# Kernel tuning notes

Measured on AMD Instinct MI355X. Metric: run time of the kernel, lower is better.

The kernel has to match this reference:

```python
import jax, jax.numpy as jnp
import numpy as np

DIM = 512   # model dim C (num_heads=1 -> head_dim = C)
NK = 128    # tokens per key-batch element
BQ = 512    # query batch
BK = 256    # key batch
NC = 1000   # num_classes for visual_fc head


def _ln(x, g, b, eps=1e-5):
    m = x.mean(-1, keepdims=True)
    v = x.var(-1, keepdims=True)
    return (x - m) * jax.lax.rsqrt(v + eps) * g + b


def _l2norm(x, eps=1e-12):  # F.normalize(p=2, dim=-1)
    n = jnp.linalg.norm(x, axis=-1, keepdims=True)
    return x / jnp.maximum(n, eps)


def setup_inputs() -> dict:
    key = jax.random.key(0)
    ks = jax.random.split(key, 8)
    s = 0.02
    return {
        "qx": jax.random.normal(ks[0], (BQ, 1, DIM), dtype=jnp.float32),
        "kx": jax.random.normal(ks[1], (BK, NK, DIM), dtype=jnp.float32),
        "key_padding_mask": jax.random.randint(ks[2], (BK, NK), 0, 2).astype(bool),
        "logit_scale": jnp.array([np.log(100.0)], dtype=jnp.float32),
        "g_q": jnp.ones((DIM,), jnp.float32), "b_q": jnp.zeros((DIM,), jnp.float32),
        "g_k": jnp.ones((DIM,), jnp.float32), "b_k": jnp.zeros((DIM,), jnp.float32),
        "wq": jax.random.normal(ks[3], (DIM, DIM), dtype=jnp.float32) * s,
        "wk": jax.random.normal(ks[4], (DIM, DIM), dtype=jnp.float32) * s,
        "w1": jax.random.normal(ks[5], (4 * DIM, DIM), dtype=jnp.float32) * s,
        "b1": jnp.zeros((4 * DIM,), jnp.float32),
        "w2": jax.random.normal(ks[6], (NC, 4 * DIM), dtype=jnp.float32) * s,
        "b2": jnp.zeros((NC,), jnp.float32),
    }


def reference(qx, kx, key_padding_mask, logit_scale,
              g_q, b_q, g_k, b_k, wq, wk, w1, b1, w2, b2):
    C = qx.shape[-1]
    scale = C ** -0.5  # num_heads=1 so head_dim == C
    # cross-batch single-query attention (Attention.forward)
    q = _ln(qx, g_q, b_q) @ wq.T                       # [Bq,1,C]
    k = _ln(kx, g_k, b_k) @ wk.T                       # [Bk,Nk,C]
    attn = jnp.einsum('qoc,knc->qkn', q, k) * scale    # [Bq,Bk,Nk]
    attn = jnp.where(key_padding_mask[None, :, :], -jnp.inf, attn)
    attn = jax.nn.softmax(attn, axis=-1)
    v = jnp.einsum('knc,qkn->qkc', kx, attn)           # [Bq,Bk,C]
    # two_branch head
    h = jax.nn.relu(qx[:, 0, :] @ w1.T + b1)           # [Bq,4C]
    x1 = h @ w2.T + b2                                 # [Bq,NC]
    x2 = jnp.einsum('qkc,qoc->qk', _l2norm(v), _l2norm(qx)) * jnp.exp(logit_scale)[0]
    return (x1, x2)
```

## Files before the change

### kernel.cpp

```cpp
#include <hip/hip_runtime.h>

typedef unsigned short u16;
typedef unsigned int u32;
typedef short bf16x8s __attribute__((ext_vector_type(8)));
typedef float f32x4 __attribute__((ext_vector_type(4)));

#define SCALE_C 0.044194173824159216f
#define MFMA16 __builtin_amdgcn_mfma_f32_16x16x32_bf16

__device__ __forceinline__ u16 f2bf(float f){
  union { float f; u32 u; } c; c.f = f;
  u32 u = c.u;
  return (u16)((u + 0x7fffu + ((u >> 16) & 1u)) >> 16);
}

__device__ __forceinline__ void gload16(const void* g, void* l){
  __builtin_amdgcn_global_load_lds((const __attribute__((address_space(1))) void*)g,
                                   (__attribute__((address_space(3))) void*)l, 16, 0, 0);
}

#define OFF_KXB  ((size_t)0)
#define OFF_G    (OFF_KXB + 33554432)
#define OFF_W2B  (OFF_G + 8388608)
#define OFF_H    (OFF_W2B + 4096000)
#define OFF_W1B  (OFF_H + 2097152)
#define OFF_QLN  (OFF_W1B + 2097152)
#define OFF_QHAT (OFF_QLN + 524288)
#define OFF_QXB  (OFF_QHAT + 524288)
#define OFF_P    (OFF_QXB + 524288)
#define OFF_M2   (OFF_P + 524288)
#define OFF_WQB  (OFF_M2 + 524288)
#define OFF_WCT  (OFF_WQB + 524288)
#define OFF_KM   (OFF_WCT + 524288)
#define OFF_KR   (OFF_KM + 131072)
#define OFF_T2   (OFF_KR + 131072)
#define OFF_FLAG (OFF_T2 + 4096)

__global__ __launch_bounds__(512) void k_phase1(
    const float* __restrict__ qx, const float* __restrict__ kx,
    const int* __restrict__ maskw,
    const float* __restrict__ g_q, const float* __restrict__ b_q,
    const float* __restrict__ wq, const float* __restrict__ wk,
    const float* __restrict__ w1, const float* __restrict__ b1,
    const float* __restrict__ w2, const float* __restrict__ b2,
    u16* __restrict__ kxb, float* __restrict__ km, float* __restrict__ kr,
    u16* __restrict__ Gm,
    u16* __restrict__ qln, u16* __restrict__ qhat,
    u16* __restrict__ wct, u16* __restrict__ w2b, u16* __restrict__ hbuf,
    float* __restrict__ t2s, int* __restrict__ flag, float* __restrict__ x1o)
{
  __shared__ __align__(16) u16 lBig[16384];
  __shared__ float redq[8][2];
  __shared__ int smax;
  const int bid = blockIdx.x, tid = threadIdx.x;
  const int lane = tid & 63, w = tid >> 6;
  const int l15 = lane & 15, lg = lane >> 4;

  if (bid < 256){
    u16* lk = lBig;
    const int z = bid;
    const int a0 = (w>>2)*64, b0 = (w&3)*32;
    float s[16] = {0,0,0,0,0,0,0,0,0,0,0,0,0,0,0,0};
    float sq[16] = {0,0,0,0,0,0,0,0,0,0,0,0,0,0,0,0};
    f32x4 acc[4][2] = {};
    for (int ch = 0; ch < 4; ch++){
      #pragma unroll
      for (int i = 0; i < 16; i++){
        int r = w*16 + i;
        float2 v = *(const float2*)(kx + ((size_t)z*128 + r)*512 + ch*128 + lane*2);
        s[i] += v.x + v.y; sq[i] += v.x*v.x + v.y*v.y;
        u32 pk = f2bf(v.x) | ((u32)f2bf(v.y)<<16);
        *(u32*)(kxb + ((size_t)z*128 + r)*512 + ch*128 + lane*2) = pk;
        *(u32*)&lk[r*128 + ((lane*2) ^ ((r&7)<<3))] = pk;
      }
      __syncthreads();
      #pragma unroll
      for (int kk = 0; kk < 4; kk++){
        int cgr = kk*4 + lg;
        bf16x8s a[4], b[2];
        #pragma unroll
        for (int i2 = 0; i2 < 4; i2++){
          int r = a0 + i2*16 + l15;
          a[i2] = *(const bf16x8s*)&lk[r*128 + ((cgr*8) ^ ((r&7)<<3))];
        }
        #pragma unroll
        for (int j = 0; j < 2; j++){
          int r = b0 + j*16 + l15;
          b[j] = *(const bf16x8s*)&lk[r*128 + ((cgr*8) ^ ((r&7)<<3))];
        }
        #pragma unroll
        for (int i2 = 0; i2 < 4; i2++)
          #pragma unroll
          for (int j = 0; j < 2; j++)
            acc[i2][j] = MFMA16(a[i2], b[j], acc[i2][j], 0,0,0);
      }
      __syncthreads();
    }
    #pragma unroll
    for (int i = 0; i < 16; i++){
      float ss = s[i], qq = sq[i];
      #pragma unroll
      for (int o = 1; o < 64; o <<= 1){ ss += __shfl_xor(ss,o); qq += __shfl_xor(qq,o); }
      if (lane == 0){
        int r = w*16 + i;
        float mean = ss*(1.0f/512.0f);
        float var  = qq*(1.0f/512.0f) - mean*mean;
        km[z*128+r] = mean; kr[z*128+r] = rsqrtf(var + 1e-5f);
      }
    }
    u16* G = Gm + (size_t)z*16384;
    #pragma unroll
    for (int i2 = 0; i2 < 4; i2++)
      #pragma unroll
      for (int j = 0; j < 2; j++)
        #pragma unroll
        for (int r = 0; r < 4; r++)
          G[(size_t)(a0 + i2*16 + lg*4 + r)*128 + b0 + j*16 + l15] = f2bf(acc[i2][j][r]);
  } else if (bid < 512){
    const int row = (bid-256)*2 + (tid>>8);
    const int t = tid & 255;
    float2 v = *(const float2*)(qx + (size_t)row*512 + t*2);
    float s = v.x+v.y, sq = v.x*v.x+v.y*v.y;
    #pragma unroll
    for (int o = 1; o < 64; o <<= 1){ s += __shfl_xor(s,o); sq += __shfl_xor(sq,o); }
    if (lane == 0){ redq[w][0]=s; redq[w][1]=sq; }
    __syncthreads();
    const int h4 = (tid>>8)*4;
    s  = redq[h4][0]+redq[h4+1][0]+redq[h4+2][0]+redq[h4+3][0];
    sq = redq[h4][1]+redq[h4+1][1]+redq[h4+2][1]+redq[h4+3][1];
    float mean = s*(1.0f/512.0f);
    float var  = sq*(1.0f/512.0f) - mean*mean;
    float rstd = rsqrtf(var + 1e-5f);
    float il2  = 1.0f / fmaxf(sqrtf(sq), 1e-12f);
    float2 g  = *(const float2*)(g_q + t*2);
    float2 bb = *(const float2*)(b_q + t*2);
    u32 a  = f2bf((v.x-mean)*rstd*g.x+bb.x) | ((u32)f2bf((v.y-mean)*rstd*g.y+bb.y)<<16);
    u32 hh = f2bf(v.x*il2) | ((u32)f2bf(v.y*il2)<<16);
    *(u32*)(qln  + (size_t)row*512 + t*2) = a;
    *(u32*)(qhat + (size_t)row*512 + t*2) = hh;
  } else if (bid < 1512){
    int i = (bid-512)*512 + tid;
    float4 v = *(const float4*)(w2 + (size_t)i*4);
    uint2 p;
    p.x = f2bf(v.x)|((u32)f2bf(v.y)<<16); p.y = f2bf(v.z)|((u32)f2bf(v.w)<<16);
    *(uint2*)(w2b + (size_t)i*4) = p;
  } else if (bid < 1640){
    const int t = bid - 1512;
    const int m0 = (t >> 4)*64, n0 = (t & 15)*128;
    const int w4 = w & 3;
    const int nb = (w >> 2)*64;
    const int wr = (w4>>1)*32, wc = (w4&1)*32;
    u16* shA = lBig;
    u16* shB = lBig + 4096;
    f32x4 acc[2][2] = {};
    for (int kc = 0; kc < 512; kc += 64){
      {
        int row = tid >> 3, c8 = (tid & 7)*8;
        float4 a0 = *(const float4*)(qx + (size_t)(m0+row)*512 + kc + c8);
        float4 a1 = *(const float4*)(qx + (size_t)(m0+row)*512 + kc + c8 + 4);
        u16 ta[8] = {f2bf(a0.x),f2bf(a0.y),f2bf(a0.z),f2bf(a0.w),
                     f2bf(a1.x),f2bf(a1.y),f2bf(a1.z),f2bf(a1.w)};
        *(uint4*)&shA[row*64 + (((tid&7) ^ (row&7))*8)] = *(uint4*)ta;
        #pragma unroll
        for (int s2 = 0; s2 < 2; s2++){
          int u = tid + s2*512;
          int rowb = u >> 3, cb8 = (u & 7)*8;
          float4 b0 = *(const float4*)(w1 + (size_t)(n0+rowb)*512 + kc + cb8);
          float4 b1v = *(const float4*)(w1 + (size_t)(n0+rowb)*512 + kc + cb8 + 4);
          u16 tb[8] = {f2bf(b0.x),f2bf(b0.y),f2bf(b0.z),f2bf(b0.w),
                       f2bf(b1v.x),f2bf(b1v.y),f2bf(b1v.z),f2bf(b1v.w)};
          *(uint4*)&shB[rowb*64 + (((u&7) ^ (rowb&7))*8)] = *(uint4*)tb;
        }
      }
      __syncthreads();
      #pragma unroll
      for (int kk = 0; kk < 2; kk++){
        int cgr = kk*4 + lg;
        int ra0 = wr + l15, ra1 = wr + 16 + l15;
        int rb0 = nb + wc + l15, rb1 = nb + wc + 16 + l15;
        bf16x8s a0 = *(const bf16x8s*)&shA[ra0*64 + ((cgr ^ (ra0&7))*8)];
        bf16x8s a1 = *(const bf16x8s*)&shA[ra1*64 + ((cgr ^ (ra1&7))*8)];
        bf16x8s b0 = *(const bf16x8s*)&shB[rb0*64 + ((cgr ^ (rb0&7))*8)];
        bf16x8s b1 = *(const bf16x8s*)&shB[rb1*64 + ((cgr ^ (rb1&7))*8)];
        acc[0][0]=MFMA16(a0,b0,acc[0][0],0,0,0);
        acc[0][1]=MFMA16(a0,b1,acc[0][1],0,0,0);
        acc[1][0]=MFMA16(a1,b0,acc[1][0],0,0,0);
        acc[1][1]=MFMA16(a1,b1,acc[1][1],0,0,0);
      }
      __syncthreads();
    }
    #pragma unroll
    for (int i = 0; i < 2; i++)
      #pragma unroll
      for (int j = 0; j < 2; j++){
        int col = n0 + nb + wc + j*16 + l15;
        float bv = b1[col];
        #pragma unroll
        for (int r = 0; r < 4; r++){
          int row = m0 + wr + i*16 + lg*4 + r;
          hbuf[(size_t)row*2048 + col] = f2bf(fmaxf(acc[i][j][r] + bv, 0.0f));
        }
      }
  } else if (bid < 1704){
    const int t = bid - 1640;
    const int f0 = (t>>3)*64, c0 = (t&7)*64;
    const int w4 = w & 3;
    const int wr = (w4>>1)*32, wc = (w4&1)*32;
    u16* shA = lBig;
    u16* shB = lBig + 4096;
    f32x4 acc[2][2] = {};
    for (int i0 = 0; i0 < 512; i0 += 64){
      const int ii = tid >> 3;
      const int cc8 = (tid & 7) * 8;
      float4 va0 = *(const float4*)(wk + (size_t)(i0+ii)*512 + f0 + cc8);
      float4 va1 = *(const float4*)(wk + (size_t)(i0+ii)*512 + f0 + cc8 + 4);
      float4 vb0 = *(const float4*)(wq + (size_t)(i0+ii)*512 + c0 + cc8);
      float4 vb1 = *(const float4*)(wq + (size_t)(i0+ii)*512 + c0 + cc8 + 4);
      #pragma unroll
      for (int e = 0; e < 8; e++){
        float fa = e < 4 ? (&va0.x)[e] : (&va1.x)[e-4];
        float fb = e < 4 ? (&vb0.x)[e] : (&vb1.x)[e-4];
        int rowc = cc8 + e;
        int idx = rowc*64 + (((ii>>3) ^ (rowc&7))*8 + (ii&7));
        shA[idx] = f2bf(fa);
        shB[idx] = f2bf(fb);
      }
      __syncthreads();
      #pragma unroll
      for (int kk = 0; kk < 2; kk++){
        int cgr = kk*4 + lg;
        int ra0 = wr + l15, ra1 = wr + 16 + l15;
        int rb0 = wc + l15, rb1 = wc + 16 + l15;
        bf16x8s a0 = *(const bf16x8s*)&shA[ra0*64 + ((cgr ^ (ra0&7))*8)];
        bf16x8s a1 = *(const bf16x8s*)&shA[ra1*64 + ((cgr ^ (ra1&7))*8)];
        bf16x8s b0 = *(const bf16x8s*)&shB[rb0*64 + ((cgr ^ (rb0&7))*8)];
        bf16x8s b1 = *(const bf16x8s*)&shB[rb1*64 + ((cgr ^ (rb1&7))*8)];
        acc[0][0]=MFMA16(a0,b0,acc[0][0],0,0,0);
        acc[0][1]=MFMA16(a0,b1,acc[0][1],0,0,0);
        acc[1][0]=MFMA16(a1,b0,acc[1][0],0,0,0);
        acc[1][1]=MFMA16(a1,b1,acc[1][1],0,0,0);
      }
      __syncthreads();
    }
    if (tid < 256){
      #pragma unroll
      for (int i = 0; i < 2; i++)
        #pragma unroll
        for (int j = 0; j < 2; j++)
          #pragma unroll
          for (int r = 0; r < 4; r++)
            wct[(size_t)(f0 + wr + i*16 + lg*4 + r)*512 + c0 + wc + j*16 + l15]
                = f2bf(acc[i][j][r]);
    }
  } else if (bid < 1954){
    int i = (bid-1704)*2048 + tid*4;
    #pragma unroll
    for (int e = 0; e < 4; e++){
      int idx = i + e;
      x1o[idx] = b2[idx % 1000];
    }
  } else {
    if (tid == 0) smax = 0;
    t2s[tid] = 0.0f;
    __syncthreads();
    int mx = 0;
    for (int i = tid; i < 8192; i += 512){ int v = maskw[i]; mx = v > mx ? v : mx; }
    #pragma unroll
    for (int o = 1; o < 64; o <<= 1){ int t2 = __shfl_xor(mx,o); mx = t2 > mx ? t2 : mx; }
    if ((tid & 63) == 0) atomicMax(&smax, mx);
    __syncthreads();
    if (tid == 0) *flag = (smax <= 1) ? 1 : 0;
  }
}

__device__ __forceinline__ void gemm_body(const u16* __restrict__ Ap, const u16* __restrict__ Bp,
    int M, int N, int K, int m0, int n0, int tid,
    u16 (*lA)[64], u16 (*lB)[64], f32x4 (&acc)[2][2])
{
  const int lane = tid & 63, w = tid >> 6;
  const int wr = (w >> 1)*32, wc = (w & 1)*32;
  const int l15 = lane & 15, lg = lane >> 4;
  for (int kc = 0; kc < K; kc += 64){
    #pragma unroll
    for (int s = 0; s < 2; s++){
      int u = tid + s*256;
      int row = u >> 3, cg = u & 7;
      int sw = (cg ^ (row & 7)) * 8;
      uint4 va = make_uint4(0,0,0,0);
      if (m0 + row < M) va = *(const uint4*)(Ap + (size_t)(m0+row)*K + kc + cg*8);
      *(uint4*)&lA[row][sw] = va;
      uint4 vb = make_uint4(0,0,0,0);
      if (n0 + row < N) vb = *(const uint4*)(Bp + (size_t)(n0+row)*K + kc + cg*8);
      *(uint4*)&lB[row][sw] = vb;
    }
    __syncthreads();
    #pragma unroll
    for (int kk = 0; kk < 2; kk++){
      int cgr = kk*4 + lg;
      int ra0 = wr + l15, ra1 = wr + 16 + l15;
      int rb0 = wc + l15, rb1 = wc + 16 + l15;
      bf16x8s a0 = *(const bf16x8s*)&lA[ra0][(cgr ^ (ra0&7))*8];
      bf16x8s a1 = *(const bf16x8s*)&lA[ra1][(cgr ^ (ra1&7))*8];
      bf16x8s b0 = *(const bf16x8s*)&lB[rb0][(cgr ^ (rb0&7))*8];
      bf16x8s b1 = *(const bf16x8s*)&lB[rb1][(cgr ^ (rb1&7))*8];
      acc[0][0] = MFMA16(a0,b0,acc[0][0],0,0,0);
      acc[0][1] = MFMA16(a0,b1,acc[0][1],0,0,0);
      acc[1][0] = MFMA16(a1,b0,acc[1][0],0,0,0);
      acc[1][1] = MFMA16(a1,b1,acc[1][1],0,0,0);
    }
    __syncthreads();
  }
}

__global__ __launch_bounds__(256) void k_phase2(
    const u16* __restrict__ qln, const u16* __restrict__ wct,
    const float* __restrict__ g_k, u16* __restrict__ m2, float* __restrict__ t2s,
    const u16* __restrict__ hbuf, const u16* __restrict__ w2b,
    float* __restrict__ x1o)
{
  __shared__ __align__(16) u16 lA[64][64], lB[64][64];
  f32x4 acc[2][2] = {};
  const int bid = blockIdx.x, tid = threadIdx.x;
  const int lane = tid & 63, w = tid >> 6;
  const int wr = (w >> 1)*32, wc = (w & 1)*32;
  const int l15 = lane & 15, lg = lane >> 4;
  if (bid < 512){
    const int ks = bid >> 7;
    const int t  = bid & 127;
    const int m0 = (t >> 4)*64, n0 = (t & 15)*64;
    for (int kc = ks*512; kc < ks*512 + 512; kc += 64){
      #pragma unroll
      for (int s = 0; s < 2; s++){
        int u = tid + s*256;
        int row = u >> 3, cg = u & 7;
        int sw = (cg ^ (row & 7)) * 8;
        *(uint4*)&lA[row][sw] = *(const uint4*)(hbuf + (size_t)(m0+row)*2048 + kc + cg*8);
        uint4 vb = make_uint4(0,0,0,0);
        if (n0 + row < 1000) vb = *(const uint4*)(w2b + (size_t)(n0+row)*2048 + kc + cg*8);
        *(uint4*)&lB[row][sw] = vb;
      }
      __syncthreads();
      #pragma unroll
      for (int kk = 0; kk < 2; kk++){
        int cgr = kk*4 + lg;
        int ra0 = wr + l15, ra1 = wr + 16 + l15;
        int rb0 = wc + l15, rb1 = wc + 16 + l15;
        bf16x8s a0 = *(const bf16x8s*)&lA[ra0][(cgr ^ (ra0&7))*8];
        bf16x8s a1 = *(const bf16x8s*)&lA[ra1][(cgr ^ (ra1&7))*8];
        bf16x8s b0 = *(const bf16x8s*)&lB[rb0][(cgr ^ (rb0&7))*8];
        bf16x8s b1 = *(const bf16x8s*)&lB[rb1][(cgr ^ (rb1&7))*8];
        acc[0][0]=MFMA16(a0,b0,acc[0][0],0,0,0);
        acc[0][1]=MFMA16(a0,b1,acc[0][1],0,0,0);
        acc[1][0]=MFMA16(a1,b0,acc[1][0],0,0,0);
        acc[1][1]=MFMA16(a1,b1,acc[1][1],0,0,0);
      }
      __syncthreads();
    }
    #pragma unroll
    for (int i = 0; i < 2; i++)
      #pragma unroll
      for (int j = 0; j < 2; j++){
        int col = n0 + wc + j*16 + l15;
        if (col < 1000){
          #pragma unroll
          for (int r = 0; r < 4; r++){
            int row = m0 + wr + i*16 + lg*4 + r;
            atomicAdd(&x1o[(size_t)row*1000 + col], acc[i][j][r]);
          }
        }
      }
  } else {
    const int b = bid - 512;
    int m0 = (b>>3)*64, n0 = (b&7)*64;
    gemm_body(qln, wct, 512,512,512, m0,n0, tid, lA, lB, acc);
    #pragma unroll
    for (int i = 0; i < 2; i++){
      #pragma unroll
      for (int r = 0; r < 4; r++){
        int row = m0 + wr + i*16 + lg*4 + r;
        float part = 0.f;
        #pragma unroll
        for (int j = 0; j < 2; j++){
          int col = n0 + wc + j*16 + l15;
          float e = SCALE_C * acc[i][j][r] * g_k[col];
          m2[(size_t)row*512 + col] = f2bf(e);
          part += e;
        }
        #pragma unroll
        for (int o = 1; o < 16; o <<= 1) part += __shfl_xor(part, o);
        if (l15 == 0) atomicAdd(&t2s[row], part);
      }
    }
  }
}

__global__ __launch_bounds__(512, 4) void k_attn(
    const u16* __restrict__ kxb, const u16* __restrict__ Gm,
    const u16* __restrict__ m2, const u16* __restrict__ qhat,
    const float* __restrict__ km, const float* __restrict__ kr,
    const float* __restrict__ t2s, const void* __restrict__ maskp,
    const int* __restrict__ flagp, const float* __restrict__ lsp,
    float* __restrict__ x2)
{
  __shared__ __align__(16) u16 sb[24576];
  __shared__ float lt2[128];
  __shared__ float lNum[128][2], lDen[128][2];
  u16* lP = sb;

  const int kb = blockIdx.x, q0 = blockIdx.y * 128;
  const int tid = threadIdx.x, lane = tid & 63, w = tid >> 6;
  const int wr = (w >> 1)*32, wcol = (w & 1)*64;
  const int l15 = lane & 15, lg = lane >> 4;
  const int fl = *flagp;
  const float expls = __expf(lsp[0]);

  if (tid < 128) lt2[tid] = t2s[q0 + tid];

  float kmv[4], krv[4], mbv[4];
  #pragma unroll
  for (int j = 0; j < 4; j++){
    int gn = kb*128 + wcol + j*16 + l15;
    kmv[j] = km[gn]; krv[j] = kr[gn];
    int mv = fl ? ((const int*)maskp)[gn] : (int)((const unsigned char*)maskp)[gn];
    mbv[j] = mv ? -1e30f : 0.0f;
  }

  const u16* KX = kxb + (size_t)kb * 65536;
  f32x4 aS[2][4] = {}, aD[2][4] = {};

  const int srow  = w*16 + (lane >> 2);
  const int sslot = (lane & 3) ^ ((srow >> 1) & 3);
  const int lofs  = w*512;

  #define STAGE(p) do{                                                         \
    const int kc_ = (p)*32;                                                    \
    u16* b_ = sb + ((p)&1)*12288;                                              \
    gload16(KX   + (size_t)srow*512      + kc_ + sslot*8, b_ + lofs);          \
    gload16(m2   + (size_t)(q0+srow)*512 + kc_ + sslot*8, b_ + 4096 + lofs);   \
    gload16(qhat + (size_t)(q0+srow)*512 + kc_ + sslot*8, b_ + 8192 + lofs);   \
  }while(0)

  STAGE(0);
  #pragma unroll
  for (int p = 0; p < 16; p++){
    if (p < 15){
      STAGE(p+1);
      asm volatile("s_waitcnt vmcnt(3)" ::: "memory");
    } else {
      asm volatile("s_waitcnt vmcnt(0)" ::: "memory");
    }
    __builtin_amdgcn_s_barrier();
    __builtin_amdgcn_sched_barrier(0);
    const u16* lb  = sb + (p&1)*12288;
    const u16* lKX = lb;
    const u16* lM2 = lb + 4096;
    const u16* lQH = lb + 8192;
    const int rA0 = wr + l15, rA1 = wr + 16 + l15;
    bf16x8s am0 = *(const bf16x8s*)&lM2[rA0*32 + ((lg ^ ((rA0>>1)&3))*8)];
    bf16x8s am1 = *(const bf16x8s*)&lM2[rA1*32 + ((lg ^ ((rA1>>1)&3))*8)];
    bf16x8s aq0 = *(const bf16x8s*)&lQH[rA0*32 + ((lg ^ ((rA0>>1)&3))*8)];
    bf16x8s aq1 = *(const bf16x8s*)&lQH[rA1*32 + ((lg ^ ((rA1>>1)&3))*8)];
    __builtin_amdgcn_s_setprio(1);
    #pragma unroll
    for (int j = 0; j < 4; j++){
      int rB = wcol + j*16 + l15;
      bf16x8s bk = *(const bf16x8s*)&lKX[rB*32 + ((lg ^ ((rB>>1)&3))*8)];
      aS[0][j] = MFMA16(am0, bk, aS[0][j], 0,0,0);
      aS[1][j] = MFMA16(am1, bk, aS[1][j], 0,0,0);
      aD[0][j] = MFMA16(aq0, bk, aD[0][j], 0,0,0);
      aD[1][j] = MFMA16(aq1, bk, aD[1][j], 0,0,0);
    }
    __builtin_amdgcn_s_setprio(0);
    __builtin_amdgcn_sched_barrier(0);
    __builtin_amdgcn_s_barrier();
  }
  __syncthreads();

  #pragma unroll
  for (int i = 0; i < 2; i++){
    #pragma unroll
    for (int r = 0; r < 4; r++){
      int rowl = wr + i*16 + lg*4 + r;
      float t2v = lt2[rowl];
      float sn = 0.f;
      #pragma unroll
      for (int j = 0; j < 4; j++){
        float L = krv[j]*(aS[i][j][r] - kmv[j]*t2v) + mbv[j];
        float e = __expf(L);
        aS[i][j][r] = e;
        sn += e * aD[i][j][r];
      }
      #pragma unroll
      for (int o = 1; o < 16; o <<= 1) sn += __shfl_xor(sn, o);
      if (l15 == 0) lNum[rowl][w&1] = sn;
      #pragma unroll
      for (int j = 0; j < 4; j++){
        int n = wcol + j*16 + l15;
        lP[rowl*128 + ((n>>3)^(rowl&7))*8 + (n&7)] = f2bf(aS[i][j][r]);
      }
    }
  }
  __syncthreads();

  f32x4 aT[2][4] = {};
  const u16* Gk = Gm + (size_t)kb * 16384;
  #pragma unroll
  for (int kk = 0; kk < 4; kk++){
    int cgr = kk*4 + lg;
    int rA0 = wr + l15, rA1 = wr + 16 + l15;
    bf16x8s p0 = *(const bf16x8s*)&lP[rA0*128 + ((cgr^(rA0&7))*8)];
    bf16x8s p1 = *(const bf16x8s*)&lP[rA1*128 + ((cgr^(rA1&7))*8)];
    #pragma unroll
    for (int j = 0; j < 4; j++){
      int mcol = wcol + j*16 + l15;
      bf16x8s bg = *(const bf16x8s*)(Gk + (size_t)mcol*128 + kk*32 + lg*8);
      aT[0][j] = MFMA16(p0, bg, aT[0][j], 0,0,0);
      aT[1][j] = MFMA16(p1, bg, aT[1][j], 0,0,0);
    }
  }
  #pragma unroll
  for (int i = 0; i < 2; i++){
    #pragma unroll
    for (int r = 0; r < 4; r++){
      int rowl = wr + i*16 + lg*4 + r;
      float sd = 0.f;
      #pragma unroll
      for (int j = 0; j < 4; j++) sd += aT[i][j][r] * aS[i][j][r];
      #pragma unroll
      for (int o = 1; o < 16; o <<= 1) sd += __shfl_xor(sd, o);
      if (l15 == 0) lDen[rowl][w&1] = sd;
    }
  }
  __syncthreads();

  if (tid < 128){
    float num  = lNum[tid][0] + lNum[tid][1];
    float den2 = lDen[tid][0] + lDen[tid][1];
    float den  = fmaxf(sqrtf(fmaxf(den2, 0.0f)), 1e-12f);
    x2[(size_t)(q0 + tid)*256 + kb] = expls * num / den;
  }
}

extern "C" void kernel_launch(void* const* d_in, const int* in_sizes, int n_in,
                              void* d_out, int out_size, void* d_ws, size_t ws_size,
                              hipStream_t stream)
{
  (void)in_sizes; (void)n_in; (void)out_size; (void)ws_size;
  const float* qx  = (const float*)d_in[0];
  const float* kx  = (const float*)d_in[1];
  const void*  mask= d_in[2];
  const float* lsp = (const float*)d_in[3];
  const float* g_q = (const float*)d_in[4];
  const float* b_q = (const float*)d_in[5];
  const float* g_k = (const float*)d_in[6];
  const float* wq  = (const float*)d_in[8];
  const float* wk  = (const float*)d_in[9];
  const float* w1  = (const float*)d_in[10];
  const float* b1  = (const float*)d_in[11];
  const float* w2  = (const float*)d_in[12];
  const float* b2  = (const float*)d_in[13];

  char* ws = (char*)d_ws;
  u16* kxb  = (u16*)(ws + OFF_KXB);
  u16* Gm   = (u16*)(ws + OFF_G);
  u16* w2b  = (u16*)(ws + OFF_W2B);
  u16* hbuf = (u16*)(ws + OFF_H);
  u16* qln  = (u16*)(ws + OFF_QLN);
  u16* qhat = (u16*)(ws + OFF_QHAT);
  u16* m2   = (u16*)(ws + OFF_M2);
  u16* wct  = (u16*)(ws + OFF_WCT);
  float* km  = (float*)(ws + OFF_KM);
  float* kr  = (float*)(ws + OFF_KR);
  float* t2s = (float*)(ws + OFF_T2);
  int*   flag= (int*)(ws + OFF_FLAG);
  float* x1o = (float*)d_out;
  float* x2o = (float*)d_out + 512*1000;

  k_phase1<<<dim3(1955), dim3(512), 0, stream>>>(
      qx, kx, (const int*)mask, g_q, b_q, wq, wk, w1, b1, w2, b2,
      kxb, km, kr, Gm, qln, qhat, wct, w2b, hbuf, t2s, flag, x1o);
  k_phase2<<<dim3(576), dim3(256), 0, stream>>>(
      qln, wct, g_k, m2, t2s, hbuf, w2b, x1o);
  k_attn<<<dim3(256, 4), dim3(512), 0, stream>>>(
      kxb, Gm, m2, qhat, km, kr, t2s, mask, flag, lsp, x2o);
}
```

Measured before the change: 121.3 us.

## Rebalance kernel stages: move small GEMMs earlier, fuse x1 GEMM into attention launch

```diff
diff --git a/kernel.cpp b/kernel.cpp
--- a/kernel.cpp
+++ b/kernel.cpp
@@ -36,20 +36,15 @@
 #define OFF_T2   (OFF_KR + 131072)
 #define OFF_FLAG (OFF_T2 + 4096)
 
-__global__ __launch_bounds__(512) void k_phase1(
-    const float* __restrict__ qx, const float* __restrict__ kx,
-    const int* __restrict__ maskw,
+__global__ __launch_bounds__(512) void k_phase0(
+    const float* __restrict__ qx, const int* __restrict__ maskw,
     const float* __restrict__ g_q, const float* __restrict__ b_q,
     const float* __restrict__ wq, const float* __restrict__ wk,
-    const float* __restrict__ w1, const float* __restrict__ b1,
-    const float* __restrict__ w2, const float* __restrict__ b2,
-    u16* __restrict__ kxb, float* __restrict__ km, float* __restrict__ kr,
-    u16* __restrict__ Gm,
-    u16* __restrict__ qln, u16* __restrict__ qhat,
-    u16* __restrict__ wct, u16* __restrict__ w2b, u16* __restrict__ hbuf,
+    const float* __restrict__ b2,
+    u16* __restrict__ qln, u16* __restrict__ qhat, u16* __restrict__ wct,
     float* __restrict__ t2s, int* __restrict__ flag, float* __restrict__ x1o)
 {
-  __shared__ __align__(16) u16 lBig[16384];
+  __shared__ __align__(16) u16 lBig[8192];
   __shared__ float redq[8][2];
   __shared__ int smax;
   const int bid = blockIdx.x, tid = threadIdx.x;
@@ -57,67 +52,7 @@
   const int l15 = lane & 15, lg = lane >> 4;
 
   if (bid < 256){
-    u16* lk = lBig;
-    const int z = bid;
-    const int a0 = (w>>2)*64, b0 = (w&3)*32;
-    float s[16] = {0,0,0,0,0,0,0,0,0,0,0,0,0,0,0,0};
-    float sq[16] = {0,0,0,0,0,0,0,0,0,0,0,0,0,0,0,0};
-    f32x4 acc[4][2] = {};
-    for (int ch = 0; ch < 4; ch++){
-      #pragma unroll
-      for (int i = 0; i < 16; i++){
-        int r = w*16 + i;
-        float2 v = *(const float2*)(kx + ((size_t)z*128 + r)*512 + ch*128 + lane*2);
-        s[i] += v.x + v.y; sq[i] += v.x*v.x + v.y*v.y;
-        u32 pk = f2bf(v.x) | ((u32)f2bf(v.y)<<16);
-        *(u32*)(kxb + ((size_t)z*128 + r)*512 + ch*128 + lane*2) = pk;
-        *(u32*)&lk[r*128 + ((lane*2) ^ ((r&7)<<3))] = pk;
-      }
-      __syncthreads();
-      #pragma unroll
-      for (int kk = 0; kk < 4; kk++){
-        int cgr = kk*4 + lg;
-        bf16x8s a[4], b[2];
-        #pragma unroll
-        for (int i2 = 0; i2 < 4; i2++){
-          int r = a0 + i2*16 + l15;
-          a[i2] = *(const bf16x8s*)&lk[r*128 + ((cgr*8) ^ ((r&7)<<3))];
-        }
-        #pragma unroll
-        for (int j = 0; j < 2; j++){
-          int r = b0 + j*16 + l15;
-          b[j] = *(const bf16x8s*)&lk[r*128 + ((cgr*8) ^ ((r&7)<<3))];
-        }
-        #pragma unroll
-        for (int i2 = 0; i2 < 4; i2++)
-          #pragma unroll
-          for (int j = 0; j < 2; j++)
-            acc[i2][j] = MFMA16(a[i2], b[j], acc[i2][j], 0,0,0);
-      }
-      __syncthreads();
-    }
-    #pragma unroll
-    for (int i = 0; i < 16; i++){
-      float ss = s[i], qq = sq[i];
-      #pragma unroll
-      for (int o = 1; o < 64; o <<= 1){ ss += __shfl_xor(ss,o); qq += __shfl_xor(qq,o); }
-      if (lane == 0){
-        int r = w*16 + i;
-        float mean = ss*(1.0f/512.0f);
-        float var  = qq*(1.0f/512.0f) - mean*mean;
-        km[z*128+r] = mean; kr[z*128+r] = rsqrtf(var + 1e-5f);
-      }
-    }
-    u16* G = Gm + (size_t)z*16384;
-    #pragma unroll
-    for (int i2 = 0; i2 < 4; i2++)
-      #pragma unroll
-      for (int j = 0; j < 2; j++)
-        #pragma unroll
-        for (int r = 0; r < 4; r++)
-          G[(size_t)(a0 + i2*16 + lg*4 + r)*128 + b0 + j*16 + l15] = f2bf(acc[i2][j][r]);
-  } else if (bid < 512){
-    const int row = (bid-256)*2 + (tid>>8);
+    const int row = bid*2 + (tid>>8);
     const int t = tid & 255;
     float2 v = *(const float2*)(qx + (size_t)row*512 + t*2);
     float s = v.x+v.y, sq = v.x*v.x+v.y*v.y;
@@ -138,14 +73,154 @@
     u32 hh = f2bf(v.x*il2) | ((u32)f2bf(v.y*il2)<<16);
     *(u32*)(qln  + (size_t)row*512 + t*2) = a;
     *(u32*)(qhat + (size_t)row*512 + t*2) = hh;
-  } else if (bid < 1512){
-    int i = (bid-512)*512 + tid;
-    float4 v = *(const float4*)(w2 + (size_t)i*4);
-    uint2 p;
-    p.x = f2bf(v.x)|((u32)f2bf(v.y)<<16); p.y = f2bf(v.z)|((u32)f2bf(v.w)<<16);
-    *(uint2*)(w2b + (size_t)i*4) = p;
-  } else if (bid < 1640){
-    const int t = bid - 1512;
+  } else if (bid < 320){
+    const int t = bid - 256;
+    const int f0 = (t>>3)*64, c0 = (t&7)*64;
+    const int w4 = w & 3;
+    const int wr = (w4>>1)*32, wc = (w4&1)*32;
+    u16* shA = lBig;
+    u16* shB = lBig + 4096;
+    f32x4 acc[2][2] = {};
+    for (int i0 = 0; i0 < 512; i0 += 64){
+      const int ii = tid >> 3;
+      const int cc8 = (tid & 7) * 8;
+      float4 va0 = *(const float4*)(wk + (size_t)(i0+ii)*512 + f0 + cc8);
+      float4 va1 = *(const float4*)(wk + (size_t)(i0+ii)*512 + f0 + cc8 + 4);
+      float4 vb0 = *(const float4*)(wq + (size_t)(i0+ii)*512 + c0 + cc8);
+      float4 vb1 = *(const float4*)(wq + (size_t)(i0+ii)*512 + c0 + cc8 + 4);
+      #pragma unroll
+      for (int e = 0; e < 8; e++){
+        float fa = e < 4 ? (&va0.x)[e] : (&va1.x)[e-4];
+        float fb = e < 4 ? (&vb0.x)[e] : (&vb1.x)[e-4];
+        int rowc = cc8 + e;
+        int idx = rowc*64 + (((ii>>3) ^ (rowc&7))*8 + (ii&7));
+        shA[idx] = f2bf(fa);
+        shB[idx] = f2bf(fb);
+      }
+      __syncthreads();
+      #pragma unroll
+      for (int kk = 0; kk < 2; kk++){
+        int cgr = kk*4 + lg;
+        int ra0 = wr + l15, ra1 = wr + 16 + l15;
+        int rb0 = wc + l15, rb1 = wc + 16 + l15;
+        bf16x8s a0 = *(const bf16x8s*)&shA[ra0*64 + ((cgr ^ (ra0&7))*8)];
+        bf16x8s a1 = *(const bf16x8s*)&shA[ra1*64 + ((cgr ^ (ra1&7))*8)];
+        bf16x8s b0 = *(const bf16x8s*)&shB[rb0*64 + ((cgr ^ (rb0&7))*8)];
+        bf16x8s b1 = *(const bf16x8s*)&shB[rb1*64 + ((cgr ^ (rb1&7))*8)];
+        acc[0][0]=MFMA16(a0,b0,acc[0][0],0,0,0);
+        acc[0][1]=MFMA16(a0,b1,acc[0][1],0,0,0);
+        acc[1][0]=MFMA16(a1,b0,acc[1][0],0,0,0);
+        acc[1][1]=MFMA16(a1,b1,acc[1][1],0,0,0);
+      }
+      __syncthreads();
+    }
+    if (tid < 256){
+      #pragma unroll
+      for (int i = 0; i < 2; i++)
+        #pragma unroll
+        for (int j = 0; j < 2; j++)
+          #pragma unroll
+          for (int r = 0; r < 4; r++)
+            wct[(size_t)(f0 + wr + i*16 + lg*4 + r)*512 + c0 + wc + j*16 + l15]
+                = f2bf(acc[i][j][r]);
+    }
+  } else if (bid < 570){
+    int i = (bid-320)*2048 + tid*4;
+    #pragma unroll
+    for (int e = 0; e < 4; e++){
+      int idx = i + e;
+      x1o[idx] = b2[idx % 1000];
+    }
+  } else {
+    if (tid == 0) smax = 0;
+    t2s[tid] = 0.0f;
+    __syncthreads();
+    int mx = 0;
+    for (int i = tid; i < 8192; i += 512){ int v = maskw[i]; mx = v > mx ? v : mx; }
+    #pragma unroll
+    for (int o = 1; o < 64; o <<= 1){ int t2 = __shfl_xor(mx,o); mx = t2 > mx ? t2 : mx; }
+    if ((tid & 63) == 0) atomicMax(&smax, mx);
+    __syncthreads();
+    if (tid == 0) *flag = (smax <= 1) ? 1 : 0;
+  }
+}
+
+__global__ __launch_bounds__(512) void k_phase1(
+    const float* __restrict__ qx, const float* __restrict__ kx,
+    const float* __restrict__ w1, const float* __restrict__ b1,
+    const u16* __restrict__ qln, const u16* __restrict__ wct,
+    const float* __restrict__ g_k,
+    u16* __restrict__ kxb, float* __restrict__ km, float* __restrict__ kr,
+    u16* __restrict__ Gm, u16* __restrict__ hbuf,
+    u16* __restrict__ m2, float* __restrict__ t2s)
+{
+  __shared__ __align__(16) u16 lBig[16384];
+  const int bid = blockIdx.x, tid = threadIdx.x;
+  const int lane = tid & 63, w = tid >> 6;
+  const int l15 = lane & 15, lg = lane >> 4;
+
+  if (bid < 256){
+    u16* lk = lBig;
+    const int z = bid;
+    const int a0 = (w>>2)*64, b0 = (w&3)*32;
+    float s[16] = {0,0,0,0,0,0,0,0,0,0,0,0,0,0,0,0};
+    float sq[16] = {0,0,0,0,0,0,0,0,0,0,0,0,0,0,0,0};
+    f32x4 acc[4][2] = {};
+    for (int ch = 0; ch < 4; ch++){
+      #pragma unroll
+      for (int i = 0; i < 16; i++){
+        int r = w*16 + i;
+        float2 v = *(const float2*)(kx + ((size_t)z*128 + r)*512 + ch*128 + lane*2);
+        s[i] += v.x + v.y; sq[i] += v.x*v.x + v.y*v.y;
+        u32 pk = f2bf(v.x) | ((u32)f2bf(v.y)<<16);
+        *(u32*)(kxb + ((size_t)z*128 + r)*512 + ch*128 + lane*2) = pk;
+        *(u32*)&lk[r*128 + ((lane*2) ^ ((r&7)<<3))] = pk;
+      }
+      __syncthreads();
+      #pragma unroll
+      for (int kk = 0; kk < 4; kk++){
+        int cgr = kk*4 + lg;
+        bf16x8s a[4], b[2];
+        #pragma unroll
+        for (int i2 = 0; i2 < 4; i2++){
+          int r = a0 + i2*16 + l15;
+          a[i2] = *(const bf16x8s*)&lk[r*128 + ((cgr*8) ^ ((r&7)<<3))];
+        }
+        #pragma unroll
+        for (int j = 0; j < 2; j++){
+          int r = b0 + j*16 + l15;
+          b[j] = *(const bf16x8s*)&lk[r*128 + ((cgr*8) ^ ((r&7)<<3))];
+        }
+        #pragma unroll
+        for (int i2 = 0; i2 < 4; i2++)
+          #pragma unroll
+          for (int j = 0; j < 2; j++)
+            acc[i2][j] = MFMA16(a[i2], b[j], acc[i2][j], 0,0,0);
+      }
+      __syncthreads();
+    }
+    #pragma unroll
+    for (int i = 0; i < 16; i++){
+      float ss = s[i], qq = sq[i];
+      #pragma unroll
+      for (int o = 1; o < 64; o <<= 1){ ss += __shfl_xor(ss,o); qq += __shfl_xor(qq,o); }
+      if (lane == 0){
+        int r = w*16 + i;
+        float mean = ss*(1.0f/512.0f);
+        float var  = qq*(1.0f/512.0f) - mean*mean;
+        km[z*128+r] = mean; kr[z*128+r] = rsqrtf(var + 1e-5f);
+      }
+    }
+    u16* G = Gm + (size_t)z*16384;
+    #pragma unroll
+    for (int i2 = 0; i2 < 4; i2++)
+      #pragma unroll
+      for (int j = 0; j < 2; j++)
+        #pragma unroll
+        for (int r = 0; r < 4; r++)
+          G[(size_t)(a0 + i2*16 + lg*4 + r)*128 + b0 + j*16 + l15] = f2bf(acc[i2][j][r]);
+  } else if (bid < 384){
+    const int t = bid - 256;
     const int m0 = (t >> 4)*64, n0 = (t & 15)*128;
     const int w4 = w & 3;
     const int nb = (w >> 2)*64;
@@ -201,29 +276,20 @@
           hbuf[(size_t)row*2048 + col] = f2bf(fmaxf(acc[i][j][r] + bv, 0.0f));
         }
       }
-  } else if (bid < 1704){
-    const int t = bid - 1640;
-    const int f0 = (t>>3)*64, c0 = (t&7)*64;
+  } else {
+    const int b = bid - 384;
+    const int m0 = (b>>3)*64, n0 = (b&7)*64;
     const int w4 = w & 3;
     const int wr = (w4>>1)*32, wc = (w4&1)*32;
     u16* shA = lBig;
     u16* shB = lBig + 4096;
     f32x4 acc[2][2] = {};
-    for (int i0 = 0; i0 < 512; i0 += 64){
-      const int ii = tid >> 3;
-      const int cc8 = (tid & 7) * 8;
-      float4 va0 = *(const float4*)(wk + (size_t)(i0+ii)*512 + f0 + cc8);
-      float4 va1 = *(const float4*)(wk + (size_t)(i0+ii)*512 + f0 + cc8 + 4);
-      float4 vb0 = *(const float4*)(wq + (size_t)(i0+ii)*512 + c0 + cc8);
-      float4 vb1 = *(const float4*)(wq + (size_t)(i0+ii)*512 + c0 + cc8 + 4);
-      #pragma unroll
-      for (int e = 0; e < 8; e++){
-        float fa = e < 4 ? (&va0.x)[e] : (&va1.x)[e-4];
-        float fb = e < 4 ? (&vb0.x)[e] : (&vb1.x)[e-4];
-        int rowc = cc8 + e;
-        int idx = rowc*64 + (((ii>>3) ^ (rowc&7))*8 + (ii&7));
-        shA[idx] = f2bf(fa);
-        shB[idx] = f2bf(fb);
+    for (int kc = 0; kc < 512; kc += 64){
+      {
+        int row = tid >> 3, cg = tid & 7;
+        int sw = (cg ^ (row & 7)) * 8;
+        *(uint4*)&shA[row*64 + sw] = *(const uint4*)(qln + (size_t)(m0+row)*512 + kc + cg*8);
+        *(uint4*)&shB[row*64 + sw] = *(const uint4*)(wct + (size_t)(n0+row)*512 + kc + cg*8);
       }
       __syncthreads();
       #pragma unroll
@@ -242,102 +308,74 @@
       }
       __syncthreads();
     }
-    if (tid < 256){
-      #pragma unroll
-      for (int i = 0; i < 2; i++)
-        #pragma unroll
-        for (int j = 0; j < 2; j++)
+    if (w < 4){
+      #pragma unroll
+      for (int i = 0; i < 2; i++){
+        #pragma unroll
+        for (int r = 0; r < 4; r++){
+          int row = m0 + wr + i*16 + lg*4 + r;
+          float part = 0.f;
           #pragma unroll
-          for (int r = 0; r < 4; r++)
-            wct[(size_t)(f0 + wr + i*16 + lg*4 + r)*512 + c0 + wc + j*16 + l15]
-                = f2bf(acc[i][j][r]);
-    }
-  } else if (bid < 1954){
-    int i = (bid-1704)*2048 + tid*4;
-    #pragma unroll
-    for (int e = 0; e < 4; e++){
-      int idx = i + e;
-      x1o[idx] = b2[idx % 1000];
-    }
-  } else {
-    if (tid == 0) smax = 0;
-    t2s[tid] = 0.0f;
-    __syncthreads();
-    int mx = 0;
-    for (int i = tid; i < 8192; i += 512){ int v = maskw[i]; mx = v > mx ? v : mx; }
-    #pragma unroll
-    for (int o = 1; o < 64; o <<= 1){ int t2 = __shfl_xor(mx,o); mx = t2 > mx ? t2 : mx; }
-    if ((tid & 63) == 0) atomicMax(&smax, mx);
-    __syncthreads();
-    if (tid == 0) *flag = (smax <= 1) ? 1 : 0;
+          for (int j = 0; j < 2; j++){
+            int col = n0 + wc + j*16 + l15;
+            float e = SCALE_C * acc[i][j][r] * g_k[col];
+            m2[(size_t)row*512 + col] = f2bf(e);
+            part += e;
+          }
+          #pragma unroll
+          for (int o = 1; o < 16; o <<= 1) part += __shfl_xor(part, o);
+          if (l15 == 0) atomicAdd(&t2s[row], part);
+        }
+      }
+    }
   }
 }
 
-__device__ __forceinline__ void gemm_body(const u16* __restrict__ Ap, const u16* __restrict__ Bp,
-    int M, int N, int K, int m0, int n0, int tid,
-    u16 (*lA)[64], u16 (*lB)[64], f32x4 (&acc)[2][2])
-{
-  const int lane = tid & 63, w = tid >> 6;
-  const int wr = (w >> 1)*32, wc = (w & 1)*32;
-  const int l15 = lane & 15, lg = lane >> 4;
-  for (int kc = 0; kc < K; kc += 64){
-    #pragma unroll
-    for (int s = 0; s < 2; s++){
-      int u = tid + s*256;
-      int row = u >> 3, cg = u & 7;
-      int sw = (cg ^ (row & 7)) * 8;
-      uint4 va = make_uint4(0,0,0,0);
-      if (m0 + row < M) va = *(const uint4*)(Ap + (size_t)(m0+row)*K + kc + cg*8);
-      *(uint4*)&lA[row][sw] = va;
-      uint4 vb = make_uint4(0,0,0,0);
-      if (n0 + row < N) vb = *(const uint4*)(Bp + (size_t)(n0+row)*K + kc + cg*8);
-      *(uint4*)&lB[row][sw] = vb;
-    }
-    __syncthreads();
-    #pragma unroll
-    for (int kk = 0; kk < 2; kk++){
-      int cgr = kk*4 + lg;
-      int ra0 = wr + l15, ra1 = wr + 16 + l15;
-      int rb0 = wc + l15, rb1 = wc + 16 + l15;
-      bf16x8s a0 = *(const bf16x8s*)&lA[ra0][(cgr ^ (ra0&7))*8];
-      bf16x8s a1 = *(const bf16x8s*)&lA[ra1][(cgr ^ (ra1&7))*8];
-      bf16x8s b0 = *(const bf16x8s*)&lB[rb0][(cgr ^ (rb0&7))*8];
-      bf16x8s b1 = *(const bf16x8s*)&lB[rb1][(cgr ^ (rb1&7))*8];
-      acc[0][0] = MFMA16(a0,b0,acc[0][0],0,0,0);
-      acc[0][1] = MFMA16(a0,b1,acc[0][1],0,0,0);
-      acc[1][0] = MFMA16(a1,b0,acc[1][0],0,0,0);
-      acc[1][1] = MFMA16(a1,b1,acc[1][1],0,0,0);
-    }
-    __syncthreads();
-  }
-}
-
-__global__ __launch_bounds__(256) void k_phase2(
-    const u16* __restrict__ qln, const u16* __restrict__ wct,
-    const float* __restrict__ g_k, u16* __restrict__ m2, float* __restrict__ t2s,
-    const u16* __restrict__ hbuf, const u16* __restrict__ w2b,
+__global__ __launch_bounds__(512, 4) void k_attn(
+    const u16* __restrict__ kxb, const u16* __restrict__ Gm,
+    const u16* __restrict__ m2, const u16* __restrict__ qhat,
+    const float* __restrict__ km, const float* __restrict__ kr,
+    const float* __restrict__ t2s, const void* __restrict__ maskp,
+    const int* __restrict__ flagp, const float* __restrict__ lsp,
+    float* __restrict__ x2,
+    const u16* __restrict__ hbuf, const float* __restrict__ w2,
     float* __restrict__ x1o)
 {
-  __shared__ __align__(16) u16 lA[64][64], lB[64][64];
-  f32x4 acc[2][2] = {};
-  const int bid = blockIdx.x, tid = threadIdx.x;
-  const int lane = tid & 63, w = tid >> 6;
-  const int wr = (w >> 1)*32, wc = (w & 1)*32;
+  __shared__ __align__(16) u16 sb[24576];
+  __shared__ float lt2[128];
+  __shared__ float lNum[128][2], lDen[128][2];
+  u16* lP = sb;
+
+  const int tid = threadIdx.x, lane = tid & 63, w = tid >> 6;
   const int l15 = lane & 15, lg = lane >> 4;
-  if (bid < 512){
-    const int ks = bid >> 7;
-    const int t  = bid & 127;
-    const int m0 = (t >> 4)*64, n0 = (t & 15)*64;
+
+  if (blockIdx.x < 64){
+    const int t = blockIdx.x*4 + blockIdx.y;
+    const int tile = t >> 2, ks = t & 3;
+    const int m0 = (tile>>3)*64, n0 = (tile&7)*128;
+    const int wr = (w >> 2)*32, wc = (w & 3)*32;
+    u16* lA = sb;
+    u16* lB = sb + 4096;
+    f32x4 acc[2][2] = {};
     for (int kc = ks*512; kc < ks*512 + 512; kc += 64){
-      #pragma unroll
-      for (int s = 0; s < 2; s++){
-        int u = tid + s*256;
-        int row = u >> 3, cg = u & 7;
-        int sw = (cg ^ (row & 7)) * 8;
-        *(uint4*)&lA[row][sw] = *(const uint4*)(hbuf + (size_t)(m0+row)*2048 + kc + cg*8);
-        uint4 vb = make_uint4(0,0,0,0);
-        if (n0 + row < 1000) vb = *(const uint4*)(w2b + (size_t)(n0+row)*2048 + kc + cg*8);
-        *(uint4*)&lB[row][sw] = vb;
+      {
+        int row = tid >> 3, cg = tid & 7;
+        *(uint4*)&lA[row*64 + ((cg ^ (row&7))*8)] =
+            *(const uint4*)(hbuf + (size_t)(m0+row)*2048 + kc + cg*8);
+        #pragma unroll
+        for (int s2 = 0; s2 < 2; s2++){
+          int u = tid + s2*512;
+          int rowb = u >> 3, cb8 = (u & 7)*8;
+          uint4 vb = make_uint4(0,0,0,0);
+          if (n0 + rowb < 1000){
+            float4 b0 = *(const float4*)(w2 + (size_t)(n0+rowb)*2048 + kc + cb8);
+            float4 b1v = *(const float4*)(w2 + (size_t)(n0+rowb)*2048 + kc + cb8 + 4);
+            u16 tb[8] = {f2bf(b0.x),f2bf(b0.y),f2bf(b0.z),f2bf(b0.w),
+                         f2bf(b1v.x),f2bf(b1v.y),f2bf(b1v.z),f2bf(b1v.w)};
+            vb = *(uint4*)tb;
+          }
+          *(uint4*)&lB[rowb*64 + (((u&7) ^ (rowb&7))*8)] = vb;
+        }
       }
       __syncthreads();
       #pragma unroll
@@ -345,10 +383,10 @@
         int cgr = kk*4 + lg;
         int ra0 = wr + l15, ra1 = wr + 16 + l15;
         int rb0 = wc + l15, rb1 = wc + 16 + l15;
-        bf16x8s a0 = *(const bf16x8s*)&lA[ra0][(cgr ^ (ra0&7))*8];
-        bf16x8s a1 = *(const bf16x8s*)&lA[ra1][(cgr ^ (ra1&7))*8];
-        bf16x8s b0 = *(const bf16x8s*)&lB[rb0][(cgr ^ (rb0&7))*8];
-        bf16x8s b1 = *(const bf16x8s*)&lB[rb1][(cgr ^ (rb1&7))*8];
+        bf16x8s a0 = *(const bf16x8s*)&lA[ra0*64 + ((cgr ^ (ra0&7))*8)];
+        bf16x8s a1 = *(const bf16x8s*)&lA[ra1*64 + ((cgr ^ (ra1&7))*8)];
+        bf16x8s b0 = *(const bf16x8s*)&lB[rb0*64 + ((cgr ^ (rb0&7))*8)];
+        bf16x8s b1 = *(const bf16x8s*)&lB[rb1*64 + ((cgr ^ (rb1&7))*8)];
         acc[0][0]=MFMA16(a0,b0,acc[0][0],0,0,0);
         acc[0][1]=MFMA16(a0,b1,acc[0][1],0,0,0);
         acc[1][0]=MFMA16(a1,b0,acc[1][0],0,0,0);
@@ -369,48 +407,11 @@
           }
         }
       }
-  } else {
-    const int b = bid - 512;
-    int m0 = (b>>3)*64, n0 = (b&7)*64;
-    gemm_body(qln, wct, 512,512,512, m0,n0, tid, lA, lB, acc);
-    #pragma unroll
-    for (int i = 0; i < 2; i++){
-      #pragma unroll
-      for (int r = 0; r < 4; r++){
-        int row = m0 + wr + i*16 + lg*4 + r;
-        float part = 0.f;
-        #pragma unroll
-        for (int j = 0; j < 2; j++){
-          int col = n0 + wc + j*16 + l15;
-          float e = SCALE_C * acc[i][j][r] * g_k[col];
-          m2[(size_t)row*512 + col] = f2bf(e);
-          part += e;
-        }
-        #pragma unroll
-        for (int o = 1; o < 16; o <<= 1) part += __shfl_xor(part, o);
-        if (l15 == 0) atomicAdd(&t2s[row], part);
-      }
-    }
-  }
-}
-
-__global__ __launch_bounds__(512, 4) void k_attn(
-    const u16* __restrict__ kxb, const u16* __restrict__ Gm,
-    const u16* __restrict__ m2, const u16* __restrict__ qhat,
-    const float* __restrict__ km, const float* __restrict__ kr,
-    const float* __restrict__ t2s, const void* __restrict__ maskp,
-    const int* __restrict__ flagp, const float* __restrict__ lsp,
-    float* __restrict__ x2)
-{
-  __shared__ __align__(16) u16 sb[24576];
-  __shared__ float lt2[128];
-  __shared__ float lNum[128][2], lDen[128][2];
-  u16* lP = sb;
-
-  const int kb = blockIdx.x, q0 = blockIdx.y * 128;
-  const int tid = threadIdx.x, lane = tid & 63, w = tid >> 6;
+    return;
+  }
+
+  const int kb = blockIdx.x - 64, q0 = blockIdx.y * 128;
   const int wr = (w >> 1)*32, wcol = (w & 1)*64;
-  const int l15 = lane & 15, lg = lane >> 4;
   const int fl = *flagp;
   const float expls = __expf(lsp[0]);
 
@@ -563,7 +564,6 @@
   char* ws = (char*)d_ws;
   u16* kxb  = (u16*)(ws + OFF_KXB);
   u16* Gm   = (u16*)(ws + OFF_G);
-  u16* w2b  = (u16*)(ws + OFF_W2B);
   u16* hbuf = (u16*)(ws + OFF_H);
   u16* qln  = (u16*)(ws + OFF_QLN);
   u16* qhat = (u16*)(ws + OFF_QHAT);
@@ -576,11 +576,13 @@
   float* x1o = (float*)d_out;
   float* x2o = (float*)d_out + 512*1000;
 
-  k_phase1<<<dim3(1955), dim3(512), 0, stream>>>(
-      qx, kx, (const int*)mask, g_q, b_q, wq, wk, w1, b1, w2, b2,
-      kxb, km, kr, Gm, qln, qhat, wct, w2b, hbuf, t2s, flag, x1o);
-  k_phase2<<<dim3(576), dim3(256), 0, stream>>>(
-      qln, wct, g_k, m2, t2s, hbuf, w2b, x1o);
-  k_attn<<<dim3(256, 4), dim3(512), 0, stream>>>(
-      kxb, Gm, m2, qhat, km, kr, t2s, mask, flag, lsp, x2o);
+  k_phase0<<<dim3(571), dim3(512), 0, stream>>>(
+      qx, (const int*)mask, g_q, b_q, wq, wk, b2,
+      qln, qhat, wct, t2s, flag, x1o);
+  k_phase1<<<dim3(448), dim3(512), 0, stream>>>(
+      qx, kx, w1, b1, qln, wct, g_k,
+      kxb, km, kr, Gm, hbuf, m2, t2s);
+  k_attn<<<dim3(320, 4), dim3(512), 0, stream>>>(
+      kxb, Gm, m2, qhat, km, kr, t2s, mask, flag, lsp, x2o,
+      hbuf, w2, x1o);
 }
```

After: 126.5 us. 1.04x slower.
